# Performance work log

Hardware: AMD Instinct MI355X
Metric: run time of the kernel (lower is better)

The kernel has to match this reference:

```python
import jax, jax.numpy as jnp
import numpy as np
from jax import lax

DEPTH = 3
KS = 5

def haar_fwd(x):
    # x: (B, 2h, 2w, C) -> (B, h, w, C, 4) with bands [LL, LH, HL, HH]
    a = x[:, 0::2, 0::2]; b = x[:, 0::2, 1::2]
    c = x[:, 1::2, 0::2]; d = x[:, 1::2, 1::2]
    ll = (a + b + c + d) * 0.5
    lh = (a + b - c - d) * 0.5
    hl = (a - b + c - d) * 0.5
    hh = (a - b - c + d) * 0.5
    return jnp.stack([ll, lh, hl, hh], axis=-1)

def haar_inv(co):
    # co: (B, h, w, C, 4) -> (B, 2h, 2w, C); orthonormal inverse of haar_fwd
    ll, lh, hl, hh = co[..., 0], co[..., 1], co[..., 2], co[..., 3]
    a = (ll + lh + hl + hh) * 0.5
    b = (ll + lh - hl - hh) * 0.5
    c = (ll - lh + hl - hh) * 0.5
    d = (ll - lh - hl + hh) * 0.5
    B, h, w, C = ll.shape
    top = jnp.stack([a, b], axis=3).reshape(B, h, 2 * w, C)
    bot = jnp.stack([c, d], axis=3).reshape(B, h, 2 * w, C)
    return jnp.stack([top, bot], axis=2).reshape(B, 2 * h, 2 * w, C)

def depthwise(x, k, groups):
    return lax.conv_general_dilated(
        x, k, (1, 1), 'SAME',
        dimension_numbers=('NHWC', 'HWIO', 'NHWC'),
        feature_group_count=groups)

def setup_inputs() -> dict:
    key = jax.random.key(0)
    ks = jax.random.split(key, 2 + DEPTH)
    B, H, W, C = 8, 256, 256, 128
    x = jax.random.normal(ks[0], (B, H, W, C), jnp.float32)
    fan = float(KS * KS)
    base_kernel = jax.random.normal(ks[1], (KS, KS, 1, C), jnp.float32) / np.sqrt(fan)
    base_bias = jnp.zeros((C,), jnp.float32)
    base_scale = jnp.ones((1, 1, 1, C), jnp.float32)
    wavelet_kernels = tuple(
        jax.random.normal(ks[2 + i], (KS, KS, 1, C * 4), jnp.float32) / np.sqrt(fan)
        for i in range(DEPTH))
    wavelet_scales = tuple(jnp.full((1, 1, 1, C * 4), 0.1, jnp.float32) for _ in range(DEPTH))
    return dict(x=x, base_kernel=base_kernel, base_bias=base_bias, base_scale=base_scale,
                wavelet_kernels=wavelet_kernels, wavelet_scales=wavelet_scales)

def reference(x, base_kernel, base_bias, base_scale, wavelet_kernels, wavelet_scales):
    B, H, W, C = x.shape
    # pad input to even H/W (edge mode); no-op for even dims
    xp = jnp.pad(x, ((0, 0), (0, H % 2), (0, W % 2), (0, 0)), mode='edge')
    # multi-level Haar forward: level l decomposes the raw LL of level l-1
    coeffs, dims = [], []
    cur = xp
    for _ in range(DEPTH):
        _, h, w, _ = cur.shape
        dims.append((h, w))
        cur = jnp.pad(cur, ((0, 0), (0, h % 2), (0, w % 2), (0, 0)), mode='edge')
        co = haar_fwd(cur)
        coeffs.append(co)
        cur = co[..., 0]
    # per-level depthwise conv with scale fused into the kernel
    conv_coeffs = []
    for lvl in range(DEPTH):
        co = coeffs[lvl]
        Bc, h, w, Cc, _ = co.shape
        flat = co.reshape(Bc, h, w, Cc * 4)
        fused = wavelet_scales[lvl] * wavelet_kernels[lvl]  # (KS,KS,1,4C)
        out = depthwise(flat, fused, Cc * 4)
        conv_coeffs.append(out.reshape(Bc, h, w, Cc, 4))
    # inverse reconstruction with add of deeper reconstruction into LL band
    next_ll = jnp.zeros_like(conv_coeffs[-1][..., 0])
    for lvl in range(DEPTH - 1, -1, -1):
        co = conv_coeffs[lvl].at[..., 0].add(next_ll)
        rec = haar_inv(co)
        h, w = dims[lvl]
        next_ll = rec[:, :h, :w, :]
    output_wt = next_ll[:, :H, :W, :]
    x_base = base_scale * (depthwise(xp, base_kernel, C) + base_bias)[:, :H, :W, :]
    return x_base + output_wt
```

## Files before the change

### kernel.cpp

```cpp
#include <hip/hip_runtime.h>

#define NC 128
#define NB 8
#define CPB 32

__device__ __forceinline__ float4 ld4(const float* p) { return *(const float4*)p; }
__device__ __forceinline__ float4 add4(float4 a, float4 b) {
    return make_float4(a.x + b.x, a.y + b.y, a.z + b.z, a.w + b.w);
}
__device__ __forceinline__ float4 sub4(float4 a, float4 b) {
    return make_float4(a.x - b.x, a.y - b.y, a.z - b.z, a.w - b.w);
}
__device__ __forceinline__ float4 muls4(float4 a, float s) {
    return make_float4(a.x * s, a.y * s, a.z * s, a.w * s);
}
__device__ __forceinline__ float4 fma4(float4 a, float4 w, float4 c) {
    return make_float4(fmaf(a.x, w.x, c.x), fmaf(a.y, w.y, c.y),
                       fmaf(a.z, w.z, c.z), fmaf(a.w, w.w, c.w));
}

__global__ __launch_bounds__(256) void k_haar_ll(
    const float* __restrict__ P, float* __restrict__ out, int h, int w)
{
    int idx = blockIdx.x * blockDim.x + threadIdx.x;
    int total = NB * h * w * (NC / 4);
    if (idx >= total) return;
    int cq = idx & (NC / 4 - 1);
    int t  = idx / (NC / 4);
    int j  = t % w; t /= w;
    int i  = t % h;
    int b  = t / h;
    size_t W2C  = (size_t)(2 * w) * NC;
    size_t base = (((size_t)b * (2 * h) + 2 * i) * (2 * w) + 2 * j) * NC + cq * 4;
    float4 A  = *(const float4*)(P + base);
    float4 Bv = *(const float4*)(P + base + NC);
    float4 Cv = *(const float4*)(P + base + W2C);
    float4 Dv = *(const float4*)(P + base + W2C + NC);
    float4 r;
    r.x = (A.x + Bv.x + Cv.x + Dv.x) * 0.5f;
    r.y = (A.y + Bv.y + Cv.y + Dv.y) * 0.5f;
    r.z = (A.z + Bv.z + Cv.z + Dv.z) * 0.5f;
    r.w = (A.w + Bv.w + Cv.w + Dv.w) * 0.5f;
    *(float4*)(out + (size_t)idx * 4) = r;
}

#define WL4(s, t)  (wl + ((s) * 25 + (t)) * CPB + 4 * tc)
#define WB4(m, n)  (wbase + ((m) * 5 + (n)) * CPB + 4 * tc)

template <bool BASE, int RR>
__global__ __launch_bounds__(256) void k_convinv(
    const float* __restrict__ P, const float* __restrict__ nll,
    const float* __restrict__ wk, const float* __restrict__ wsc,
    const float* __restrict__ bk, const float* __restrict__ bb,
    const float* __restrict__ bs, float* __restrict__ out,
    int h, int w)
{
    extern __shared__ float lds[];
    float* wl     = lds;
    float* wbase  = wl + 4 * 25 * CPB;
    float* bscale = wbase + 25 * CPB;
    float* bbias  = bscale + CPB;

    const int cg    = blockIdx.x & 3;
    const int jtile = blockIdx.x >> 2;
    const int c0    = cg * CPB;
    const int tid   = threadIdx.x + threadIdx.y * 8;

    for (int u = tid; u < 4 * 25 * CPB; u += 256) {
        int tcc = u & (CPB - 1);
        int st  = u / CPB;
        int t   = st % 25;
        int s   = st / 25;
        wl[u] = 0.5f * wsc[(c0 + tcc) * 4 + s] * wk[t * (4 * NC) + (c0 + tcc) * 4 + s];
    }
    if (BASE) {
        for (int u = tid; u < 25 * CPB; u += 256) {
            int tcc = u & (CPB - 1);
            int t   = u / CPB;
            wbase[u] = bk[t * NC + c0 + tcc];
        }
        if (tid < CPB) { bscale[tid] = bs[c0 + tid]; bbias[tid] = bb[c0 + tid]; }
    }
    __syncthreads();

    const int tc = threadIdx.x;
    const int cc = c0 + 4 * tc;
    const int b  = blockIdx.z;
    const int i  = blockIdx.y;
    const int ja = jtile * (32 * RR) + threadIdx.y * RR;
    if (ja >= w) return;
    const int PH = 2 * h;
    const size_t rowC = (size_t)(2 * w) * NC;

    float4 nv[RR];
    #pragma unroll
    for (int s = 0; s < RR; ++s) {
        int j = ja + s;
        nv[s] = (nll && j < w)
              ? ld4(nll + (((size_t)b * h + i) * w + j) * NC + cc)
              : make_float4(0.f, 0.f, 0.f, 0.f);
    }

    int   coff[RR + 4];
    float cmask[RR + 4];
    #pragma unroll
    for (int q = 0; q < RR + 4; ++q) {
        int xq  = ja + q - 2;
        int xqc = min(max(xq, 0), w - 1);
        coff[q]  = xqc * (2 * NC);
        cmask[q] = (xq >= 0 && xq < w) ? 1.f : 0.f;
    }

    float4 acc0[RR], acc1[RR], acc2[RR], acc3[RR];
    float4 b00[RR], b01[RR], b10[RR], b11[RR];
    #pragma unroll
    for (int s = 0; s < RR; ++s) {
        acc0[s] = acc1[s] = acc2[s] = acc3[s] = make_float4(0.f, 0.f, 0.f, 0.f);
        b00[s] = b01[s] = b10[s] = b11[s] = make_float4(0.f, 0.f, 0.f, 0.f);
    }

    #pragma unroll
    for (int ky = 0; ky < 5; ++ky) {
        int y = i + ky - 2;
        if (y < 0 || y >= h) continue;
        const float* prA = P + ((size_t)b * PH + 2 * y) * rowC + cc;
        const float* prC = prA + rowC;
        #pragma unroll
        for (int q = 0; q < RR + 4; ++q) {
            float m = cmask[q];
            const float* pA = prA + coff[q];
            const float* pC = prC + coff[q];
            float4 A  = muls4(ld4(pA), m);
            float4 Bv = muls4(ld4(pA + NC), m);
            float4 Cv = muls4(ld4(pC), m);
            float4 Dv = muls4(ld4(pC + NC), m);
            float4 sA = add4(A, Bv), sC = add4(Cv, Dv);
            float4 dA = sub4(A, Bv), dC = sub4(Cv, Dv);
            float4 s0 = add4(sA, sC), s1 = sub4(sA, sC);
            float4 s2 = add4(dA, dC), s3 = sub4(dA, dC);
            #pragma unroll
            for (int s = 0; s < RR; ++s) {
                const int kx = q - s;
                if (kx < 0 || kx > 4) continue;
                const int t = ky * 5 + kx;
                acc0[s] = fma4(s0, ld4(WL4(0, t)), acc0[s]);
                acc1[s] = fma4(s1, ld4(WL4(1, t)), acc1[s]);
                acc2[s] = fma4(s2, ld4(WL4(2, t)), acc2[s]);
                acc3[s] = fma4(s3, ld4(WL4(3, t)), acc3[s]);
                if (BASE && ky >= 1 && ky <= 3 && kx >= 1 && kx <= 3) {
                    b00[s] = fma4(A, ld4(WB4(2 * ky - 2, 2 * kx - 2)), b00[s]);
                    if (kx >= 2)            b01[s] = fma4(A,  ld4(WB4(2 * ky - 2, 2 * kx - 3)), b01[s]);
                    if (ky >= 2)            b10[s] = fma4(A,  ld4(WB4(2 * ky - 3, 2 * kx - 2)), b10[s]);
                    if (ky >= 2 && kx >= 2) b11[s] = fma4(A,  ld4(WB4(2 * ky - 3, 2 * kx - 3)), b11[s]);
                    if (kx <= 2)            b00[s] = fma4(Bv, ld4(WB4(2 * ky - 2, 2 * kx - 1)), b00[s]);
                                            b01[s] = fma4(Bv, ld4(WB4(2 * ky - 2, 2 * kx - 2)), b01[s]);
                    if (ky >= 2 && kx <= 2) b10[s] = fma4(Bv, ld4(WB4(2 * ky - 3, 2 * kx - 1)), b10[s]);
                    if (ky >= 2)            b11[s] = fma4(Bv, ld4(WB4(2 * ky - 3, 2 * kx - 2)), b11[s]);
                    if (ky <= 2)            b00[s] = fma4(Cv, ld4(WB4(2 * ky - 1, 2 * kx - 2)), b00[s]);
                    if (ky <= 2 && kx >= 2) b01[s] = fma4(Cv, ld4(WB4(2 * ky - 1, 2 * kx - 3)), b01[s]);
                                            b10[s] = fma4(Cv, ld4(WB4(2 * ky - 2, 2 * kx - 2)), b10[s]);
                    if (kx >= 2)            b11[s] = fma4(Cv, ld4(WB4(2 * ky - 2, 2 * kx - 3)), b11[s]);
                    if (ky <= 2 && kx <= 2) b00[s] = fma4(Dv, ld4(WB4(2 * ky - 1, 2 * kx - 1)), b00[s]);
                    if (ky <= 2)            b01[s] = fma4(Dv, ld4(WB4(2 * ky - 1, 2 * kx - 2)), b01[s]);
                    if (kx <= 2)            b10[s] = fma4(Dv, ld4(WB4(2 * ky - 2, 2 * kx - 1)), b10[s]);
                                            b11[s] = fma4(Dv, ld4(WB4(2 * ky - 2, 2 * kx - 2)), b11[s]);
                }
            }
        }
    }

    #pragma unroll
    for (int s = 0; s < RR; ++s) {
        int j = ja + s;
        if (j >= w) break;
        float4 a0 = add4(acc0[s], nv[s]);
        float4 av = muls4(add4(add4(a0, acc1[s]), add4(acc2[s], acc3[s])), 0.5f);
        float4 bv = muls4(sub4(add4(a0, acc1[s]), add4(acc2[s], acc3[s])), 0.5f);
        float4 cv = muls4(add4(sub4(a0, acc1[s]), sub4(acc2[s], acc3[s])), 0.5f);
        float4 dv = muls4(sub4(sub4(a0, acc1[s]), sub4(acc2[s], acc3[s])), 0.5f);

        size_t ob = ((size_t)b * PH + 2 * i) * rowC + (size_t)(2 * j) * NC + cc;
        if (BASE) {
            float4 sc = ld4(bscale + 4 * tc);
            float4 bi = ld4(bbias + 4 * tc);
            float4 o00 = make_float4(sc.x * (b00[s].x + bi.x), sc.y * (b00[s].y + bi.y),
                                     sc.z * (b00[s].z + bi.z), sc.w * (b00[s].w + bi.w));
            float4 o01 = make_float4(sc.x * (b01[s].x + bi.x), sc.y * (b01[s].y + bi.y),
                                     sc.z * (b01[s].z + bi.z), sc.w * (b01[s].w + bi.w));
            float4 o10 = make_float4(sc.x * (b10[s].x + bi.x), sc.y * (b10[s].y + bi.y),
                                     sc.z * (b10[s].z + bi.z), sc.w * (b10[s].w + bi.w));
            float4 o11 = make_float4(sc.x * (b11[s].x + bi.x), sc.y * (b11[s].y + bi.y),
                                     sc.z * (b11[s].z + bi.z), sc.w * (b11[s].w + bi.w));
            *(float4*)(out + ob)             = add4(o00, av);
            *(float4*)(out + ob + NC)        = add4(o01, bv);
            *(float4*)(out + ob + rowC)      = add4(o10, cv);
            *(float4*)(out + ob + rowC + NC) = add4(o11, dv);
        } else {
            *(float4*)(out + ob)             = av;
            *(float4*)(out + ob + NC)        = bv;
            *(float4*)(out + ob + rowC)      = cv;
            *(float4*)(out + ob + rowC + NC) = dv;
        }
    }
}

extern "C" void kernel_launch(void* const* d_in, const int* in_sizes, int n_in,
                              void* d_out, int out_size, void* d_ws, size_t ws_size,
                              hipStream_t stream)
{
    const float* x  = (const float*)d_in[0];
    const float* bk = (const float*)d_in[1];
    const float* bb = (const float*)d_in[2];
    const float* bs = (const float*)d_in[3];
    const float* wk[3];
    const float* wv[3];
    if (n_in >= 10) {
        for (int i = 0; i < 3; ++i) {
            wk[i] = (const float*)d_in[4 + i];
            wv[i] = (const float*)d_in[7 + i];
        }
    } else {
        const float* wkc = (const float*)d_in[4];
        const float* wvc = (const float*)d_in[5];
        for (int i = 0; i < 3; ++i) {
            wk[i] = wkc + (size_t)i * 25 * 4 * NC;
            wv[i] = wvc + (size_t)i * 4 * NC;
        }
    }
    float* out = (float*)d_out;

    float* ll0 = out;
    float* ll1 = out + 16777216;
    float* r2  = out + 16777216 + 4194304;
    float* r1  = (float*)d_ws;

    {
        int total = NB * 128 * 128 * (NC / 4);
        k_haar_ll<<<(total + 255) / 256, 256, 0, stream>>>(x, ll0, 128, 128);
    }
    {
        int total = NB * 64 * 64 * (NC / 4);
        k_haar_ll<<<(total + 255) / 256, 256, 0, stream>>>(ll0, ll1, 64, 64);
    }

    size_t lds_nb = (size_t)(4 * 25 * CPB) * sizeof(float);
    size_t lds_b  = (size_t)(4 * 25 * CPB + 25 * CPB + 2 * CPB) * sizeof(float);
    dim3 blk(8, 32);

    k_convinv<false, 1><<<dim3(4, 32, NB), blk, lds_nb, stream>>>(
        ll1, nullptr, wk[2], wv[2], nullptr, nullptr, nullptr, r2, 32, 32);

    k_convinv<false, 2><<<dim3(4, 64, NB), blk, lds_nb, stream>>>(
        ll0, r2, wk[1], wv[1], nullptr, nullptr, nullptr, r1, 64, 64);

    k_convinv<true, 1><<<dim3(4 * 4, 128, NB), blk, lds_b, stream>>>(
        x, r1, wk[0], wv[0], bk, bb, bs, out, 128, 128);
}
```

Baseline: 557.5 us.

## Move base-conv accumulation after wavelet loop and raise outputs per thread

The base 5x5 depthwise conv accumulators (b00..b11 per output) are no longer kept live through the wavelet conv loop. They are computed per output column after it, re-reading the 3x3 neighbourhood of 2x2 input blocks, with a sched_barrier separating the two phases. This cuts register pressure, which allows RR=2 outputs per thread for the finest level and halves the grid in x. The cost is reloading input pixels (cache hits) for the base conv and extra live state from the doubled RR.

```diff
diff --git a/kernel.cpp b/kernel.cpp
--- a/kernel.cpp
+++ b/kernel.cpp
@@ -112,12 +112,9 @@
     }
 
     float4 acc0[RR], acc1[RR], acc2[RR], acc3[RR];
-    float4 b00[RR], b01[RR], b10[RR], b11[RR];
-    #pragma unroll
-    for (int s = 0; s < RR; ++s) {
+    #pragma unroll
+    for (int s = 0; s < RR; ++s)
         acc0[s] = acc1[s] = acc2[s] = acc3[s] = make_float4(0.f, 0.f, 0.f, 0.f);
-        b00[s] = b01[s] = b10[s] = b11[s] = make_float4(0.f, 0.f, 0.f, 0.f);
-    }
 
     #pragma unroll
     for (int ky = 0; ky < 5; ++ky) {
@@ -147,27 +144,11 @@
                 acc1[s] = fma4(s1, ld4(WL4(1, t)), acc1[s]);
                 acc2[s] = fma4(s2, ld4(WL4(2, t)), acc2[s]);
                 acc3[s] = fma4(s3, ld4(WL4(3, t)), acc3[s]);
-                if (BASE && ky >= 1 && ky <= 3 && kx >= 1 && kx <= 3) {
-                    b00[s] = fma4(A, ld4(WB4(2 * ky - 2, 2 * kx - 2)), b00[s]);
-                    if (kx >= 2)            b01[s] = fma4(A,  ld4(WB4(2 * ky - 2, 2 * kx - 3)), b01[s]);
-                    if (ky >= 2)            b10[s] = fma4(A,  ld4(WB4(2 * ky - 3, 2 * kx - 2)), b10[s]);
-                    if (ky >= 2 && kx >= 2) b11[s] = fma4(A,  ld4(WB4(2 * ky - 3, 2 * kx - 3)), b11[s]);
-                    if (kx <= 2)            b00[s] = fma4(Bv, ld4(WB4(2 * ky - 2, 2 * kx - 1)), b00[s]);
-                                            b01[s] = fma4(Bv, ld4(WB4(2 * ky - 2, 2 * kx - 2)), b01[s]);
-                    if (ky >= 2 && kx <= 2) b10[s] = fma4(Bv, ld4(WB4(2 * ky - 3, 2 * kx - 1)), b10[s]);
-                    if (ky >= 2)            b11[s] = fma4(Bv, ld4(WB4(2 * ky - 3, 2 * kx - 2)), b11[s]);
-                    if (ky <= 2)            b00[s] = fma4(Cv, ld4(WB4(2 * ky - 1, 2 * kx - 2)), b00[s]);
-                    if (ky <= 2 && kx >= 2) b01[s] = fma4(Cv, ld4(WB4(2 * ky - 1, 2 * kx - 3)), b01[s]);
-                                            b10[s] = fma4(Cv, ld4(WB4(2 * ky - 2, 2 * kx - 2)), b10[s]);
-                    if (kx >= 2)            b11[s] = fma4(Cv, ld4(WB4(2 * ky - 2, 2 * kx - 3)), b11[s]);
-                    if (ky <= 2 && kx <= 2) b00[s] = fma4(Dv, ld4(WB4(2 * ky - 1, 2 * kx - 1)), b00[s]);
-                    if (ky <= 2)            b01[s] = fma4(Dv, ld4(WB4(2 * ky - 1, 2 * kx - 2)), b01[s]);
-                    if (kx <= 2)            b10[s] = fma4(Dv, ld4(WB4(2 * ky - 2, 2 * kx - 1)), b10[s]);
-                                            b11[s] = fma4(Dv, ld4(WB4(2 * ky - 2, 2 * kx - 2)), b11[s]);
-                }
             }
         }
     }
+
+    if (BASE) __builtin_amdgcn_sched_barrier(0);
 
     #pragma unroll
     for (int s = 0; s < RR; ++s) {
@@ -181,16 +162,52 @@
 
         size_t ob = ((size_t)b * PH + 2 * i) * rowC + (size_t)(2 * j) * NC + cc;
         if (BASE) {
+            float4 b00 = make_float4(0.f, 0.f, 0.f, 0.f);
+            float4 b01 = b00, b10 = b00, b11 = b00;
+            #pragma unroll
+            for (int ky = 1; ky <= 3; ++ky) {
+                int y = i + ky - 2;
+                if (y < 0 || y >= h) continue;
+                const float* prA = P + ((size_t)b * PH + 2 * y) * rowC + cc;
+                const float* prC = prA + rowC;
+                #pragma unroll
+                for (int kx = 1; kx <= 3; ++kx) {
+                    const int q = s + kx;
+                    float m = cmask[q];
+                    const float* pA = prA + coff[q];
+                    const float* pC = prC + coff[q];
+                    float4 A  = muls4(ld4(pA), m);
+                    float4 Bv = muls4(ld4(pA + NC), m);
+                    float4 Cv = muls4(ld4(pC), m);
+                    float4 Dv = muls4(ld4(pC + NC), m);
+                    b00 = fma4(A, ld4(WB4(2 * ky - 2, 2 * kx - 2)), b00);
+                    if (kx >= 2)            b01 = fma4(A,  ld4(WB4(2 * ky - 2, 2 * kx - 3)), b01);
+                    if (ky >= 2)            b10 = fma4(A,  ld4(WB4(2 * ky - 3, 2 * kx - 2)), b10);
+                    if (ky >= 2 && kx >= 2) b11 = fma4(A,  ld4(WB4(2 * ky - 3, 2 * kx - 3)), b11);
+                    if (kx <= 2)            b00 = fma4(Bv, ld4(WB4(2 * ky - 2, 2 * kx - 1)), b00);
+                                            b01 = fma4(Bv, ld4(WB4(2 * ky - 2, 2 * kx - 2)), b01);
+                    if (ky >= 2 && kx <= 2) b10 = fma4(Bv, ld4(WB4(2 * ky - 3, 2 * kx - 1)), b10);
+                    if (ky >= 2)            b11 = fma4(Bv, ld4(WB4(2 * ky - 3, 2 * kx - 2)), b11);
+                    if (ky <= 2)            b00 = fma4(Cv, ld4(WB4(2 * ky - 1, 2 * kx - 2)), b00);
+                    if (ky <= 2 && kx >= 2) b01 = fma4(Cv, ld4(WB4(2 * ky - 1, 2 * kx - 3)), b01);
+                                            b10 = fma4(Cv, ld4(WB4(2 * ky - 2, 2 * kx - 2)), b10);
+                    if (kx >= 2)            b11 = fma4(Cv, ld4(WB4(2 * ky - 2, 2 * kx - 3)), b11);
+                    if (ky <= 2 && kx <= 2) b00 = fma4(Dv, ld4(WB4(2 * ky - 1, 2 * kx - 1)), b00);
+                    if (ky <= 2)            b01 = fma4(Dv, ld4(WB4(2 * ky - 1, 2 * kx - 2)), b01);
+                    if (kx <= 2)            b10 = fma4(Dv, ld4(WB4(2 * ky - 2, 2 * kx - 1)), b10);
+                                            b11 = fma4(Dv, ld4(WB4(2 * ky - 2, 2 * kx - 2)), b11);
+                }
+            }
             float4 sc = ld4(bscale + 4 * tc);
             float4 bi = ld4(bbias + 4 * tc);
-            float4 o00 = make_float4(sc.x * (b00[s].x + bi.x), sc.y * (b00[s].y + bi.y),
-                                     sc.z * (b00[s].z + bi.z), sc.w * (b00[s].w + bi.w));
-            float4 o01 = make_float4(sc.x * (b01[s].x + bi.x), sc.y * (b01[s].y + bi.y),
-                                     sc.z * (b01[s].z + bi.z), sc.w * (b01[s].w + bi.w));
-            float4 o10 = make_float4(sc.x * (b10[s].x + bi.x), sc.y * (b10[s].y + bi.y),
-                                     sc.z * (b10[s].z + bi.z), sc.w * (b10[s].w + bi.w));
-            float4 o11 = make_float4(sc.x * (b11[s].x + bi.x), sc.y * (b11[s].y + bi.y),
-                                     sc.z * (b11[s].z + bi.z), sc.w * (b11[s].w + bi.w));
+            float4 o00 = make_float4(sc.x * (b00.x + bi.x), sc.y * (b00.y + bi.y),
+                                     sc.z * (b00.z + bi.z), sc.w * (b00.w + bi.w));
+            float4 o01 = make_float4(sc.x * (b01.x + bi.x), sc.y * (b01.y + bi.y),
+                                     sc.z * (b01.z + bi.z), sc.w * (b01.w + bi.w));
+            float4 o10 = make_float4(sc.x * (b10.x + bi.x), sc.y * (b10.y + bi.y),
+                                     sc.z * (b10.z + bi.z), sc.w * (b10.w + bi.w));
+            float4 o11 = make_float4(sc.x * (b11.x + bi.x), sc.y * (b11.y + bi.y),
+                                     sc.z * (b11.z + bi.z), sc.w * (b11.w + bi.w));
             *(float4*)(out + ob)             = add4(o00, av);
             *(float4*)(out + ob + NC)        = add4(o01, bv);
             *(float4*)(out + ob + rowC)      = add4(o10, cv);
@@ -253,6 +270,6 @@
     k_convinv<false, 2><<<dim3(4, 64, NB), blk, lds_nb, stream>>>(
         ll0, r2, wk[1], wv[1], nullptr, nullptr, nullptr, r1, 64, 64);
 
-    k_convinv<true, 1><<<dim3(4 * 4, 128, NB), blk, lds_b, stream>>>(
+    k_convinv<true, 2><<<dim3(2 * 4, 128, NB), blk, lds_b, stream>>>(
         x, r1, wk[0], wv[0], bk, bb, bs, out, 128, 128);
 }
```

New measurement: 564.5 us. No clear change (+1.3%).
